# Performance work log

Measured on AMD Instinct MI355X. Metric: run time of the kernel, lower is better.

The kernel has to match this reference:

```python
import jax, jax.numpy as jnp
import numpy as np

SIG_EPS = 0.1
IN_DIM = 256
OUT_DIM = 64


def setup_inputs() -> dict:
    key = jax.random.key(0)
    ks = jax.random.split(key, 6)
    B, S, Q = 32, 512, 512
    return {
        "phi_support": jax.random.normal(ks[0], (B, S, IN_DIM), jnp.float32),
        "y_support": jax.random.normal(ks[1], (B, S, OUT_DIM), jnp.float32),
        "phi_query": jax.random.normal(ks[2], (B, Q, IN_DIM), jnp.float32),
        "y_query": jax.random.normal(ks[3], (B, Q, OUT_DIM), jnp.float32),
        # learned parameters (K init'd to zeros in torch, use small randn for a non-trivial test)
        "K": jax.random.normal(ks[4], (IN_DIM, OUT_DIM), jnp.float32) * 0.02,
        "L_asym": jax.random.normal(ks[5], (IN_DIM, IN_DIM), jnp.float32) * 0.1,
    }


def reference(phi_support, y_support, phi_query, y_query, K, L_asym):
    sig_eps = jnp.float32(SIG_EPS)
    log_sig_eps = jnp.log(sig_eps)
    out_dim = K.shape[1]

    L = L_asym @ L_asym.T  # [I, I]
    # nobs > 0 branch (n_support = 512)
    posterior_L = jnp.einsum('bsi,bsj->bij', phi_support, phi_support) + L[None]  # [B,I,I]
    posterior_L_inv = jnp.linalg.inv(posterior_L)
    rhs = jnp.einsum('bsi,bso->bio', phi_support, y_support) + (L @ K)[None]  # [B,I,O]
    posterior_K = posterior_L_inv @ rhs  # [B,I,O]

    mu_pred = phi_query @ posterior_K  # [B,Q,O]
    # spread_fac = 1 + diag quadratic form phi Linv phi^T  -> [B,Q]
    spread_fac = 1.0 + jnp.einsum('bqi,bij,bqj->bq', phi_query, posterior_L_inv, phi_query)
    eye_eps = jnp.eye(out_dim, dtype=phi_query.dtype) * sig_eps
    sig_pred = spread_fac[..., None, None] * eye_eps  # [B,Q,O,O]

    # predictive_nll: inverse of sig_pred is an exactly scaled identity, so the
    # quadratic form y^T inv(sig_pred) y == ||y||^2 / (spread_fac * sig_eps) (same math)
    diff = y_query - mu_pred
    quadf = jnp.sum(diff * diff, axis=-1) / (spread_fac * sig_eps)  # [B,Q]
    logdet = out_dim * (jnp.log(spread_fac) + log_sig_eps)  # [B,Q]
    predictive_nll = logdet.mean() + quadf.mean()

    return (mu_pred, sig_pred, predictive_nll)
```

## Files before the change

kernel.cpp:

```cpp
#include <hip/hip_runtime.h>
#include <math.h>

#define B 32
#define S 512
#define Q 512
#define I 256
#define O 64
#define SIG_EPS 0.1f
#define LOG_SIG_EPS (-2.3025850929940457f)

#define WS_L 0
#define WS_T1 65536
#define WS_LKT 81920
#define WS_M0 98304
#define WS_M1 2195456
#define WS_RHST 4292608
#define WS_D 4816896
#define WS_SP 5079040
#define WS_NLL 5095424
#define WS_U16 5095488
#define U_PTH 0
#define U_PTL 4194304
#define U_YTH 8388608
#define U_YTL 9437184
#define U_IVH 10485760
#define U_IVL 12582912
#define U_PKH 14680064
#define U_PKL 15204352

#define OUT_MU_ELEMS (B * Q * O)
#define OUT_SIG_ELEMS (B * Q * O * O)
#define OUT_NLL_IDX (OUT_MU_ELEMS + OUT_SIG_ELEMS)

typedef short short8 __attribute__((ext_vector_type(8)));
typedef float f32x4 __attribute__((ext_vector_type(4)));
#define MFMA16(a, b, c) __builtin_amdgcn_mfma_f32_16x16x32_bf16(a, b, c, 0, 0, 0)

__device__ __forceinline__ f32x4 mfma3(short8 ah, short8 al, short8 bh, short8 bl, f32x4 c) {
  c = MFMA16(ah, bh, c);
  c = MFMA16(ah, bl, c);
  c = MFMA16(al, bh, c);
  return c;
}

__device__ __forceinline__ unsigned short f2bf(float x) {
  unsigned int u = __float_as_uint(x);
  return (unsigned short)((u + 0x7fffu + ((u >> 16) & 1u)) >> 16);
}
__device__ __forceinline__ float bf2f(unsigned short h) { return __uint_as_float(((unsigned int)h) << 16); }
__device__ __forceinline__ void split2(float x, unsigned short& h, unsigned short& l) {
  h = f2bf(x);
  l = f2bf(x - bf2f(h));
}
__device__ __forceinline__ void split4(float4 v, uint2& H, uint2& L) {
  unsigned short h0, h1, h2, h3, l0, l1, l2, l3;
  split2(v.x, h0, l0); split2(v.y, h1, l1); split2(v.z, h2, l2); split2(v.w, h3, l3);
  H.x = (unsigned)h0 | ((unsigned)h1 << 16); H.y = (unsigned)h2 | ((unsigned)h3 << 16);
  L.x = (unsigned)l0 | ((unsigned)l1 << 16); L.y = (unsigned)l2 | ((unsigned)l3 << 16);
}
__device__ __forceinline__ void cvt8(const float* p, short8& h8, short8& l8) {
  float4 a = *(const float4*)p;
  float4 b = *(const float4*)(p + 4);
  uint2 H0, L0, H1, L1;
  split4(a, H0, L0); split4(b, H1, L1);
  union { uint2 q[2]; short8 s; } uh, ul;
  uh.q[0] = H0; uh.q[1] = H1; ul.q[0] = L0; ul.q[1] = L1;
  h8 = uh.s; l8 = ul.s;
}
__device__ __forceinline__ short8 ld8(const unsigned short* p) { return *(const short8*)(const void*)p; }

__device__ __forceinline__ void fma4x4(const float4 av, const float4 bv, float acc[4][4]) {
  const float ar[4] = {av.x, av.y, av.z, av.w};
  const float br[4] = {bv.x, bv.y, bv.z, bv.w};
#pragma unroll
  for (int i = 0; i < 4; ++i)
#pragma unroll
    for (int j = 0; j < 4; ++j) acc[i][j] += ar[i] * br[j];
}

__device__ __forceinline__ void load_direct64(float* dst, int ds, const float* src, int ss, int t) {
#pragma unroll
  for (int m = 0; m < 4; ++m) {
    int r = (t >> 4) + 16 * m, c4 = (t & 15) * 4;
    *(float4*)&dst[r * ds + c4] = *(const float4*)&src[(size_t)r * ss + c4];
  }
}
__device__ __forceinline__ void load_trans64(float* dst, int ds, const float* src, int ss, int t) {
#pragma unroll
  for (int m = 0; m < 4; ++m) {
    int r = (t >> 4) + 16 * m, c4 = (t & 15) * 4;
    float4 v = *(const float4*)&src[(size_t)r * ss + c4];
    dst[(c4 + 0) * ds + r] = v.x;
    dst[(c4 + 1) * ds + r] = v.y;
    dst[(c4 + 2) * ds + r] = v.z;
    dst[(c4 + 3) * ds + r] = v.w;
  }
}
template <int SA, int SB>
__device__ __forceinline__ void gemm64(const float* At, const float* Bs, int tr, int tc, float acc[4][4]) {
#pragma unroll 8
  for (int kk = 0; kk < 64; ++kk) {
    float4 a = *(const float4*)&At[kk * SA + tr * 4];
    float4 b = *(const float4*)&Bs[kk * SB + tc * 4];
    fma4x4(a, b, acc);
  }
}

#define SC4(V) V.x *= pivinv; V.y *= pivinv; V.z *= pivinv; V.w *= pivinv
#define UP4(V, R) V.x -= g * R.x; V.y -= g * R.y; V.z -= g * R.z; V.w -= g * R.w

template <int TS>
__device__ void gj64(const float* T, float* rowbuf, float* Dout, int t) {
  int r = t >> 2, q = t & 3;
  int lane = t & 63;
  float4 A0 = *(const float4*)&T[r * TS + q * 16 + 0];
  float4 A1 = *(const float4*)&T[r * TS + q * 16 + 4];
  float4 A2 = *(const float4*)&T[r * TS + q * 16 + 8];
  float4 A3 = *(const float4*)&T[r * TS + q * 16 + 12];
#define IC(c) (((q * 16 + (c)) == r) ? 1.f : 0.f)
  float4 I0 = make_float4(IC(0), IC(1), IC(2), IC(3));
  float4 I1 = make_float4(IC(4), IC(5), IC(6), IC(7));
  float4 I2 = make_float4(IC(8), IC(9), IC(10), IC(11));
  float4 I3 = make_float4(IC(12), IC(13), IC(14), IC(15));
#undef IC
  for (int p = 0; p < 64; ++p) {
    float* RA = rowbuf + (p & 1) * 128;
    float* RI = RA + 64;
    if (r == p) {
      ((float4*)&RA[q * 16])[0] = A0; ((float4*)&RA[q * 16])[1] = A1;
      ((float4*)&RA[q * 16])[2] = A2; ((float4*)&RA[q * 16])[3] = A3;
      ((float4*)&RI[q * 16])[0] = I0; ((float4*)&RI[q * 16])[1] = I1;
      ((float4*)&RI[q * 16])[2] = I2; ((float4*)&RI[q * 16])[3] = I3;
    }
    __syncthreads();
    float pivinv = 1.0f / RA[p];
    int s = p & 15;
    float4 blk = (s < 8) ? ((s < 4) ? A0 : A1) : ((s < 12) ? A2 : A3);
    int sc = s & 3;
    float ap = (sc == 0) ? blk.x : (sc == 1) ? blk.y : (sc == 2) ? blk.z : blk.w;
    float f = __shfl(ap, (lane & ~3) | (p >> 4), 64);
    float4 ra0 = ((const float4*)&RA[q * 16])[0], ra1 = ((const float4*)&RA[q * 16])[1];
    float4 ra2 = ((const float4*)&RA[q * 16])[2], ra3 = ((const float4*)&RA[q * 16])[3];
    float4 ri0 = ((const float4*)&RI[q * 16])[0], ri1 = ((const float4*)&RI[q * 16])[1];
    float4 ri2 = ((const float4*)&RI[q * 16])[2], ri3 = ((const float4*)&RI[q * 16])[3];
    if (r == p) {
      SC4(A0); SC4(A1); SC4(A2); SC4(A3);
      SC4(I0); SC4(I1); SC4(I2); SC4(I3);
    } else {
      float g = f * pivinv;
      UP4(A0, ra0); UP4(A1, ra1); UP4(A2, ra2); UP4(A3, ra3);
      UP4(I0, ri0); UP4(I1, ri1); UP4(I2, ri2); UP4(I3, ri3);
    }
  }
  ((float4*)&Dout[r * 64 + q * 16])[0] = I0;
  ((float4*)&Dout[r * 64 + q * 16])[1] = I1;
  ((float4*)&Dout[r * 64 + q * 16])[2] = I2;
  ((float4*)&Dout[r * 64 + q * 16])[3] = I3;
}

__global__ __launch_bounds__(256) void k_cvt(const float* __restrict__ phi_s, const float* __restrict__ y_s,
                                             unsigned short* __restrict__ PTh, unsigned short* __restrict__ PTl,
                                             unsigned short* __restrict__ YTh, unsigned short* __restrict__ YTl,
                                             float* __restrict__ nllacc) {
  __shared__ unsigned short Hs[64][68];
  __shared__ unsigned short Lo[64][68];
  int blk = blockIdx.x, t = threadIdx.x;
  if (blk == 0 && t == 0) nllacc[0] = 0.f;
  const float* src;
  unsigned short *dh, *dl;
  int sstride;
  if (blk < 1024) {
    int b = blk >> 5, r = blk & 31, ic = r >> 3, sc = r & 7;
    src = phi_s + ((size_t)b * 512 + sc * 64) * 256 + ic * 64;
    sstride = 256;
    size_t d0 = ((size_t)b * 256 + ic * 64) * 512 + sc * 64;
    dh = PTh + d0; dl = PTl + d0;
  } else {
    int qq = blk - 1024, b = qq >> 3, sc = qq & 7;
    src = y_s + ((size_t)b * 512 + sc * 64) * 64;
    sstride = 64;
    size_t d0 = ((size_t)b * 64) * 512 + sc * 64;
    dh = YTh + d0; dl = YTl + d0;
  }
  int c = t & 63, rb = (t >> 6) * 16;
#pragma unroll
  for (int m = 0; m < 16; ++m) {
    int s = rb + m;
    float x = src[(size_t)s * sstride + c];
    unsigned short h, l;
    split2(x, h, l);
    Hs[c][s] = h;
    Lo[c][s] = l;
  }
  __syncthreads();
  int il0 = t >> 4, c4 = (t & 15) * 4;
#pragma unroll
  for (int m = 0; m < 4; ++m) {
    int il = il0 + 16 * m;
    uint2 H, L;
    H.x = (unsigned)Hs[il][c4] | ((unsigned)Hs[il][c4 + 1] << 16);
    H.y = (unsigned)Hs[il][c4 + 2] | ((unsigned)Hs[il][c4 + 3] << 16);
    L.x = (unsigned)Lo[il][c4] | ((unsigned)Lo[il][c4 + 1] << 16);
    L.y = (unsigned)Lo[il][c4 + 2] | ((unsigned)Lo[il][c4 + 3] << 16);
    *(uint2*)&dh[(size_t)il * 512 + c4] = H;
    *(uint2*)&dl[(size_t)il * 512 + c4] = L;
  }
}

__global__ __launch_bounds__(256) void k_pre1(const float* __restrict__ La, const float* __restrict__ Km,
                                              float* __restrict__ Lm, float* __restrict__ T1) {
  __shared__ float sA[16 * 68];
  __shared__ float sB[16 * 68];
  int blk = blockIdx.x, t = threadIdx.x;
  int tr = t >> 4, tc = t & 15;
  float acc[4][4] = {};
  if (blk < 16) {
    int i0 = (blk >> 2) * 64, j0 = (blk & 3) * 64;
    for (int ks = 0; ks < 256; ks += 16) {
      __syncthreads();
#pragma unroll
      for (int m = 0; m < 4; ++m) {
        int r = (t >> 4) + 16 * m, kk = t & 15;
        sA[kk * 68 + r] = La[(size_t)(i0 + r) * 256 + ks + kk];
        sB[kk * 68 + r] = La[(size_t)(j0 + r) * 256 + ks + kk];
      }
      __syncthreads();
#pragma unroll
      for (int kk = 0; kk < 16; ++kk) {
        float4 a = *(const float4*)&sA[kk * 68 + tr * 4];
        float4 bv = *(const float4*)&sB[kk * 68 + tc * 4];
        fma4x4(a, bv, acc);
      }
    }
#pragma unroll
    for (int mi = 0; mi < 4; ++mi) {
      float4 v = {acc[mi][0], acc[mi][1], acc[mi][2], acc[mi][3]};
      *(float4*)&Lm[(size_t)(i0 + tr * 4 + mi) * 256 + j0 + tc * 4] = v;
    }
  } else {
    int i0 = (blk - 16) * 64;
    for (int ks = 0; ks < 256; ks += 16) {
      __syncthreads();
#pragma unroll
      for (int m = 0; m < 4; ++m) {
        int kk = (t >> 6) + 4 * m, c = t & 63;
        sA[kk * 68 + c] = La[(size_t)(ks + kk) * 256 + i0 + c];
        sB[kk * 68 + c] = Km[(size_t)(ks + kk) * 64 + c];
      }
      __syncthreads();
#pragma unroll
      for (int kk = 0; kk < 16; ++kk) {
        float4 a = *(const float4*)&sA[kk * 68 + tr * 4];
        float4 bv = *(const float4*)&sB[kk * 68 + tc * 4];
        fma4x4(a, bv, acc);
      }
    }
#pragma unroll
    for (int mi = 0; mi < 4; ++mi) {
      float4 v = {acc[mi][0], acc[mi][1], acc[mi][2], acc[mi][3]};
      *(float4*)&T1[(size_t)(i0 + tr * 4 + mi) * 64 + tc * 4] = v;
    }
  }
}

__global__ __launch_bounds__(256) void k_gram(
    const unsigned short* __restrict__ PTh, const unsigned short* __restrict__ PTl,
    const unsigned short* __restrict__ YTh, const unsigned short* __restrict__ YTl,
    const float* __restrict__ Lm, const float* __restrict__ La, const float* __restrict__ T1,
    float* __restrict__ M0, float* __restrict__ RHST, float* __restrict__ LKT, float* __restrict__ Dbuf) {
  __shared__ float trbuf[64 * 68];
  __shared__ float rowbuf[256];
  __shared__ float Ws[16 * 64];
  int b = blockIdx.x, y = blockIdx.y, t = threadIdx.x;

  if (y == 14) {
    if (b >= 4) return;
    int i0 = b * 64;
    int tr = t >> 4, tc = t & 15;
    float acc[4][4] = {};
    for (int ks = 0; ks < 256; ks += 16) {
      __syncthreads();
#pragma unroll
      for (int m = 0; m < 4; ++m) {
        trbuf[(t & 15) * 68 + (t >> 4) + 16 * m] = La[(size_t)(i0 + (t >> 4) + 16 * m) * 256 + ks + (t & 15)];
        Ws[((t >> 6) + 4 * m) * 64 + (t & 63)] = T1[(size_t)(ks + (t >> 6) + 4 * m) * 64 + (t & 63)];
      }
      __syncthreads();
#pragma unroll
      for (int kk = 0; kk < 16; ++kk) {
        float4 a = *(const float4*)&trbuf[kk * 68 + tr * 4];
        float4 bv = *(const float4*)&Ws[kk * 64 + tc * 4];
        fma4x4(a, bv, acc);
      }
    }
    __syncthreads();
#pragma unroll
    for (int mi = 0; mi < 4; ++mi)
#pragma unroll
      for (int cj = 0; cj < 4; ++cj) trbuf[(tr * 4 + mi) * 68 + tc * 4 + cj] = acc[mi][cj];
    __syncthreads();
    int rr0 = t >> 4, cc4 = (t & 15) * 4;
#pragma unroll
    for (int m = 0; m < 4; ++m) {
      int rr = rr0 + 16 * m;
      float4 v = {trbuf[(cc4 + 0) * 68 + rr], trbuf[(cc4 + 1) * 68 + rr], trbuf[(cc4 + 2) * 68 + rr],
                  trbuf[(cc4 + 3) * 68 + rr]};
      *(float4*)&LKT[(size_t)rr * 256 + i0 + cc4] = v;
    }
    return;
  }

  const int TIa[14] = {0, 0, 0, 0, 1, 1, 1, 2, 2, 3, 0, 1, 2, 3};
  const int TJa[14] = {0, 1, 2, 3, 1, 2, 3, 2, 3, 3, 0, 0, 0, 0};
  bool isR = (y >= 10);
  int it = TIa[y], jt = TJa[y];
  int i0 = it * 64, j0 = isR ? 0 : jt * 64;
  int lane = t & 63, w = t >> 6, wr = w >> 1, wc = w & 1;
  const unsigned short* Ah = PTh + (size_t)b * 256 * 512;
  const unsigned short* Al = PTl + (size_t)b * 256 * 512;
  const unsigned short* Bh = isR ? (YTh + (size_t)b * 64 * 512) : Ah;
  const unsigned short* Bl = isR ? (YTl + (size_t)b * 64 * 512) : Al;
  int ra0 = i0 + wr * 32 + (lane & 15);
  int rb0 = j0 + wc * 32 + (lane & 15);
  int klane = (lane >> 4) * 8;
  f32x4 acc[2][2] = {};
  for (int ks = 0; ks < 512; ks += 32) {
    int kk = ks + klane;
    short8 a0h = ld8(Ah + (size_t)ra0 * 512 + kk);
    short8 a1h = ld8(Ah + (size_t)(ra0 + 16) * 512 + kk);
    short8 a0l = ld8(Al + (size_t)ra0 * 512 + kk);
    short8 a1l = ld8(Al + (size_t)(ra0 + 16) * 512 + kk);
    short8 b0h = ld8(Bh + (size_t)rb0 * 512 + kk);
    short8 b1h = ld8(Bh + (size_t)(rb0 + 16) * 512 + kk);
    short8 b0l = ld8(Bl + (size_t)rb0 * 512 + kk);
    short8 b1l = ld8(Bl + (size_t)(rb0 + 16) * 512 + kk);
    acc[0][0] = mfma3(a0h, a0l, b0h, b0l, acc[0][0]);
    acc[0][1] = mfma3(a0h, a0l, b1h, b1l, acc[0][1]);
    acc[1][0] = mfma3(a1h, a1l, b0h, b0l, acc[1][0]);
    acc[1][1] = mfma3(a1h, a1l, b1h, b1l, acc[1][1]);
  }
#pragma unroll
  for (int ti = 0; ti < 2; ++ti)
#pragma unroll
    for (int tj = 0; tj < 2; ++tj)
#pragma unroll
      for (int r = 0; r < 4; ++r)
        trbuf[(wr * 32 + ti * 16 + (lane >> 4) * 4 + r) * 68 + wc * 32 + tj * 16 + (lane & 15)] = acc[ti][tj][r];
  __syncthreads();
  int rr0 = t >> 4, cc4 = (t & 15) * 4;
  if (!isR) {
    float* Mb = M0 + (size_t)b * 65536;
    bool d00 = (it == 0 && jt == 0);
#pragma unroll
    for (int m = 0; m < 4; ++m) {
      int rr = rr0 + 16 * m;
      float4 v = *(float4*)&trbuf[rr * 68 + cc4];
      float4 lv = *(const float4*)&Lm[(size_t)(i0 + rr) * 256 + j0 + cc4];
      v.x += lv.x; v.y += lv.y; v.z += lv.z; v.w += lv.w;
      *(float4*)&Mb[(size_t)(i0 + rr) * 256 + j0 + cc4] = v;
      if (d00) *(float4*)&trbuf[rr * 68 + cc4] = v;
    }
    if (it != jt) {
#pragma unroll
      for (int m = 0; m < 4; ++m) {
        int rr = rr0 + 16 * m;
        float4 v = {trbuf[(cc4 + 0) * 68 + rr], trbuf[(cc4 + 1) * 68 + rr], trbuf[(cc4 + 2) * 68 + rr],
                    trbuf[(cc4 + 3) * 68 + rr]};
        float4 lv = *(const float4*)&Lm[(size_t)(j0 + rr) * 256 + i0 + cc4];
        v.x += lv.x; v.y += lv.y; v.z += lv.z; v.w += lv.w;
        *(float4*)&Mb[(size_t)(j0 + rr) * 256 + i0 + cc4] = v;
      }
    }
    if (d00) {
      __syncthreads();
      gj64<68>(trbuf, rowbuf, Dbuf + (size_t)b * 4096, t);
    }
  } else {
#pragma unroll
    for (int m = 0; m < 4; ++m) {
      int rr = rr0 + 16 * m;
      float4 v = {trbuf[(cc4 + 0) * 68 + rr], trbuf[(cc4 + 1) * 68 + rr], trbuf[(cc4 + 2) * 68 + rr],
                  trbuf[(cc4 + 3) * 68 + rr]};
      *(float4*)&RHST[((size_t)b * 64 + rr) * 256 + i0 + cc4] = v;
    }
  }
}

__global__ __launch_bounds__(256) void k_step(const float* __restrict__ Msrc_, float* __restrict__ Mdst_,
                                              float* __restrict__ Dbuf, unsigned short* __restrict__ IVh,
                                              unsigned short* __restrict__ IVl, int kb) {
  __shared__ float shA[64 * 68];
  __shared__ float shB[64 * 64];
  __shared__ float shC[64 * 64];
  __shared__ float shD[64 * 68];
  __shared__ float rowbuf[256];
  int b = blockIdx.x, u = blockIdx.y;
  int i = u >> 2, j = u & 3;
  int t = threadIdx.x;
  int tr = t >> 4, tc = t & 15;
  const float* Ms = Msrc_ + (size_t)b * 65536;
  float* Md = Mdst_ + (size_t)b * 65536;
  const float* Din = Dbuf + (size_t)(kb & 1) * (B * 4096) + (size_t)b * 4096;
  float* Dout = Dbuf + (size_t)((kb + 1) & 1) * (B * 4096) + (size_t)b * 4096;
  bool last = (kb == 3);
  unsigned short* Yh = IVh + (size_t)b * 65536;
  unsigned short* Yl = IVl + (size_t)b * 65536;
  auto STORE = [&](int row, int col, float4 v) {
    if (last) {
      uint2 H, L;
      split4(v, H, L);
      *(uint2*)&Yh[(size_t)row * 256 + col] = H;
      *(uint2*)&Yl[(size_t)row * 256 + col] = L;
    } else {
      *(float4*)&Md[(size_t)row * 256 + col] = v;
    }
  };
  bool ik = (i == kb), jk = (j == kb);
  if (ik && jk) {
#pragma unroll
    for (int m = 0; m < 4; ++m) {
      int r = (t >> 4) + 16 * m, c4 = (t & 15) * 4;
      STORE(kb * 64 + r, kb * 64 + c4, *(const float4*)&Din[r * 64 + c4]);
    }
    return;
  }
  float acc[4][4] = {};
  if (ik) {
    load_trans64(shA, 68, Din, 64, t);
    load_direct64(shB, 64, &Ms[(size_t)(kb * 64) * 256 + j * 64], 256, t);
    __syncthreads();
    gemm64<68, 64>(shA, shB, tr, tc, acc);
#pragma unroll
    for (int mi = 0; mi < 4; ++mi) {
      float4 v = {acc[mi][0], acc[mi][1], acc[mi][2], acc[mi][3]};
      STORE(kb * 64 + tr * 4 + mi, j * 64 + tc * 4, v);
    }
    return;
  }
  if (jk) {
    load_trans64(shA, 68, &Ms[(size_t)(i * 64) * 256 + kb * 64], 256, t);
    load_direct64(shB, 64, Din, 64, t);
    __syncthreads();
    gemm64<68, 64>(shA, shB, tr, tc, acc);
#pragma unroll
    for (int mi = 0; mi < 4; ++mi) {
      float4 v = {-acc[mi][0], -acc[mi][1], -acc[mi][2], -acc[mi][3]};
      STORE(i * 64 + tr * 4 + mi, kb * 64 + tc * 4, v);
    }
    return;
  }
  load_trans64(shA, 68, Din, 64, t);
  load_direct64(shB, 64, &Ms[(size_t)(kb * 64) * 256 + j * 64], 256, t);
  load_trans64(shD, 68, &Ms[(size_t)(i * 64) * 256 + kb * 64], 256, t);
  __syncthreads();
  gemm64<68, 64>(shA, shB, tr, tc, acc);
#pragma unroll
  for (int mi = 0; mi < 4; ++mi) {
    float4 v = {acc[mi][0], acc[mi][1], acc[mi][2], acc[mi][3]};
    *(float4*)&shC[(tr * 4 + mi) * 64 + tc * 4] = v;
  }
  __syncthreads();
  float acc2[4][4] = {};
  gemm64<68, 64>(shD, shC, tr, tc, acc2);
  bool la = (kb < 3) && (i == kb + 1) && (j == kb + 1);
#pragma unroll
  for (int mi = 0; mi < 4; ++mi) {
    size_t off = (size_t)(i * 64 + tr * 4 + mi) * 256 + j * 64 + tc * 4;
    float4 old = *(const float4*)&Ms[off];
    float4 v = {old.x - acc2[mi][0], old.y - acc2[mi][1], old.z - acc2[mi][2], old.w - acc2[mi][3]};
    STORE(i * 64 + tr * 4 + mi, j * 64 + tc * 4, v);
    if (la) *(float4*)&shB[(tr * 4 + mi) * 64 + tc * 4] = v;
  }
  if (la) {
    __syncthreads();
    gj64<64>(shB, rowbuf, Dout, t);
  }
}

__global__ __launch_bounds__(256) void k_postK(const unsigned short* __restrict__ IVh,
                                               const unsigned short* __restrict__ IVl,
                                               const float* __restrict__ RHST, const float* __restrict__ LKT,
                                               unsigned short* __restrict__ PKh, unsigned short* __restrict__ PKl) {
  int b = blockIdx.x, i0 = blockIdx.y * 64, t = threadIdx.x;
  int lane = t & 63, w = t >> 6, wr = w >> 1, wc = w & 1;
  const unsigned short* Ah = IVh + (size_t)b * 65536;
  const unsigned short* Al = IVl + (size_t)b * 65536;
  int ra0 = i0 + wr * 32 + (lane & 15);
  int ob0 = wc * 32 + (lane & 15);
  int klane = (lane >> 4) * 8;
  f32x4 acc[2][2] = {};
  for (int ks = 0; ks < 256; ks += 32) {
    int kk = ks + klane;
    short8 a0h = ld8(Ah + (size_t)ra0 * 256 + kk);
    short8 a1h = ld8(Ah + (size_t)(ra0 + 16) * 256 + kk);
    short8 a0l = ld8(Al + (size_t)ra0 * 256 + kk);
    short8 a1l = ld8(Al + (size_t)(ra0 + 16) * 256 + kk);
    short8 bh[2], bl[2];
#pragma unroll
    for (int s = 0; s < 2; ++s) {
      int o = ob0 + s * 16;
      float g[8];
      float4 g0 = *(const float4*)&RHST[((size_t)b * 64 + o) * 256 + kk];
      float4 g1 = *(const float4*)&RHST[((size_t)b * 64 + o) * 256 + kk + 4];
      float4 l0 = *(const float4*)&LKT[(size_t)o * 256 + kk];
      float4 l1 = *(const float4*)&LKT[(size_t)o * 256 + kk + 4];
      g[0] = g0.x + l0.x; g[1] = g0.y + l0.y; g[2] = g0.z + l0.z; g[3] = g0.w + l0.w;
      g[4] = g1.x + l1.x; g[5] = g1.y + l1.y; g[6] = g1.z + l1.z; g[7] = g1.w + l1.w;
      cvt8(g, bh[s], bl[s]);
    }
    acc[0][0] = mfma3(a0h, a0l, bh[0], bl[0], acc[0][0]);
    acc[0][1] = mfma3(a0h, a0l, bh[1], bl[1], acc[0][1]);
    acc[1][0] = mfma3(a1h, a1l, bh[0], bl[0], acc[1][0]);
    acc[1][1] = mfma3(a1h, a1l, bh[1], bl[1], acc[1][1]);
  }
#pragma unroll
  for (int ti = 0; ti < 2; ++ti)
#pragma unroll
    for (int tj = 0; tj < 2; ++tj) {
      int ib = i0 + wr * 32 + ti * 16 + (lane >> 4) * 4;
      int o = wc * 32 + tj * 16 + (lane & 15);
      float4 v = {acc[ti][tj][0], acc[ti][tj][1], acc[ti][tj][2], acc[ti][tj][3]};
      uint2 H, L;
      split4(v, H, L);
      *(uint2*)&PKh[((size_t)b * 64 + o) * 256 + ib] = H;
      *(uint2*)&PKl[((size_t)b * 64 + o) * 256 + ib] = L;
    }
}

__global__ __launch_bounds__(256) void k_musp(const float* __restrict__ phi_q,
                                              const unsigned short* __restrict__ IVh,
                                              const unsigned short* __restrict__ IVl,
                                              const unsigned short* __restrict__ PKh,
                                              const unsigned short* __restrict__ PKl, float* __restrict__ mu,
                                              float* __restrict__ spread) {
  int b = blockIdx.x, qb = blockIdx.y * 64, t = threadIdx.x;
  int lane = t & 63, w = t >> 6;
  int qs = qb + w * 16;
  int qlane = qs + (lane & 15);
  int klane = (lane >> 4) * 8;
  const float* Pq = phi_q + (size_t)b * 512 * 256;
  short8 ah[8], al[8];
#pragma unroll
  for (int k8 = 0; k8 < 8; ++k8) cvt8(&Pq[(size_t)qlane * 256 + k8 * 32 + klane], ah[k8], al[k8]);
  const unsigned short* Kh = PKh + (size_t)b * 64 * 256;
  const unsigned short* Kl = PKl + (size_t)b * 64 * 256;
#pragma unroll
  for (int ot = 0; ot < 4; ++ot) {
    f32x4 acc = {};
    int orow = ot * 16 + (lane & 15);
#pragma unroll
    for (int k8 = 0; k8 < 8; ++k8) {
      short8 bh = ld8(Kh + (size_t)orow * 256 + k8 * 32 + klane);
      short8 bl = ld8(Kl + (size_t)orow * 256 + k8 * 32 + klane);
      acc = mfma3(ah[k8], al[k8], bh, bl, acc);
    }
#pragma unroll
    for (int r = 0; r < 4; ++r)
      mu[((size_t)b * 512 + qs + (lane >> 4) * 4 + r) * 64 + ot * 16 + (lane & 15)] = acc[r];
  }
  const unsigned short* Vh = IVh + (size_t)b * 65536;
  const unsigned short* Vl = IVl + (size_t)b * 65536;
  float rs[4] = {0.f, 0.f, 0.f, 0.f};
  for (int jt = 0; jt < 16; ++jt) {
    f32x4 acc = {};
    int jrow = jt * 16 + (lane & 15);
#pragma unroll
    for (int k8 = 0; k8 < 8; ++k8) {
      short8 bh = ld8(Vh + (size_t)jrow * 256 + k8 * 32 + klane);
      short8 bl = ld8(Vl + (size_t)jrow * 256 + k8 * 32 + klane);
      acc = mfma3(ah[k8], al[k8], bh, bl, acc);
    }
#pragma unroll
    for (int r = 0; r < 4; ++r) {
      int q = qs + (lane >> 4) * 4 + r;
      rs[r] += acc[r] * Pq[(size_t)q * 256 + jt * 16 + (lane & 15)];
    }
  }
#pragma unroll
  for (int off = 1; off < 16; off <<= 1)
#pragma unroll
    for (int r = 0; r < 4; ++r) rs[r] += __shfl_xor(rs[r], off);
  if ((lane & 15) == 0) {
#pragma unroll
    for (int r = 0; r < 4; ++r) spread[(size_t)b * 512 + qs + (lane >> 4) * 4 + r] = 1.0f + rs[r];
  }
}

__global__ __launch_bounds__(256) void k_signll(const float* __restrict__ spread, float4* __restrict__ sig,
                                                const float* __restrict__ yq, const float* __restrict__ mu,
                                                float* __restrict__ nllacc) {
  int t = threadIdx.x;
  if (blockIdx.x < 65536) {
    size_t idx = (size_t)blockIdx.x * 256 + t;
    int p4 = (int)(idx & 15);
    int o = (int)((idx >> 4) & 63);
    size_t bq = idx >> 10;
    float sv = spread[bq] * SIG_EPS;
    float4 v;
    v.x = (p4 * 4 + 0 == o) ? sv : 0.f;
    v.y = (p4 * 4 + 1 == o) ? sv : 0.f;
    v.z = (p4 * 4 + 2 == o) ? sv : 0.f;
    v.w = (p4 * 4 + 3 == o) ? sv : 0.f;
    sig[idx] = v;
  } else {
    int bq = (blockIdx.x - 65536) * 256 + t;
    float sp = spread[bq];
    const float4* yv = (const float4*)(yq + (size_t)bq * 64);
    const float4* mv = (const float4*)(mu + (size_t)bq * 64);
    float ssd = 0.f;
#pragma unroll
    for (int i = 0; i < 16; ++i) {
      float4 a = yv[i], b = mv[i];
      float dx = a.x - b.x, dy = a.y - b.y, dz = a.z - b.z, dw = a.w - b.w;
      ssd += dx * dx + dy * dy + dz * dz + dw * dw;
    }
    float quadf = ssd / (sp * SIG_EPS);
    float ld = 64.0f * (logf(sp) + LOG_SIG_EPS);
    float val = (ld + quadf) * (1.0f / 16384.0f);
#pragma unroll
    for (int off = 32; off; off >>= 1) val += __shfl_down(val, off);
    if ((t & 63) == 0) atomicAdd(nllacc, val);
  }
}

__global__ void k_fin(const float* __restrict__ nllacc, float* __restrict__ out) {
  if (threadIdx.x == 0 && blockIdx.x == 0) out[0] = nllacc[0];
}

extern "C" void kernel_launch(void* const* d_in, const int* in_sizes, int n_in, void* d_out, int out_size,
                              void* d_ws, size_t ws_size, hipStream_t stream) {
  const float* phi_s = (const float*)d_in[0];
  const float* y_s = (const float*)d_in[1];
  const float* phi_q = (const float*)d_in[2];
  const float* y_q = (const float*)d_in[3];
  const float* Km = (const float*)d_in[4];
  const float* La = (const float*)d_in[5];

  float* ws = (float*)d_ws;
  float* Lm = ws + WS_L;
  float* T1 = ws + WS_T1;
  float* LKT = ws + WS_LKT;
  float* M0 = ws + WS_M0;
  float* M1 = ws + WS_M1;
  float* RHST = ws + WS_RHST;
  float* Dbuf = ws + WS_D;
  float* spread = ws + WS_SP;
  float* nllacc = ws + WS_NLL;
  unsigned short* u16b = (unsigned short*)(ws + WS_U16);
  unsigned short* PTh = u16b + U_PTH;
  unsigned short* PTl = u16b + U_PTL;
  unsigned short* YTh = u16b + U_YTH;
  unsigned short* YTl = u16b + U_YTL;
  unsigned short* IVh = u16b + U_IVH;
  unsigned short* IVl = u16b + U_IVL;
  unsigned short* PKh = u16b + U_PKH;
  unsigned short* PKl = u16b + U_PKL;

  float* out_mu = (float*)d_out;
  float* out_sig = out_mu + OUT_MU_ELEMS;
  float* out_nll = out_mu + OUT_NLL_IDX;

  k_cvt<<<1280, 256, 0, stream>>>(phi_s, y_s, PTh, PTl, YTh, YTl, nllacc);
  k_pre1<<<20, 256, 0, stream>>>(La, Km, Lm, T1);
  k_gram<<<dim3(B, 15), 256, 0, stream>>>(PTh, PTl, YTh, YTl, Lm, La, T1, M0, RHST, LKT, Dbuf);
  k_step<<<dim3(B, 16), 256, 0, stream>>>(M0, M1, Dbuf, IVh, IVl, 0);
  k_step<<<dim3(B, 16), 256, 0, stream>>>(M1, M0, Dbuf, IVh, IVl, 1);
  k_step<<<dim3(B, 16), 256, 0, stream>>>(M0, M1, Dbuf, IVh, IVl, 2);
  k_step<<<dim3(B, 16), 256, 0, stream>>>(M1, M0, Dbuf, IVh, IVl, 3);
  k_postK<<<dim3(B, 4), 256, 0, stream>>>(IVh, IVl, RHST, LKT, PKh, PKl);
  k_musp<<<dim3(B, 8), 256, 0, stream>>>(phi_q, IVh, IVl, PKh, PKl, out_mu, spread);
  k_signll<<<65600, 256, 0, stream>>>(spread, (float4*)out_sig, y_q, out_mu, nllacc);
  k_fin<<<1, 64, 0, stream>>>(nllacc, out_nll);
}
```

Baseline: 336.0 us.

## Fuse all stages into one cooperative persistent kernel with grid syncs

Replaces the chain of eleven kernel launches with a single cooperative kernel of 256 persistent blocks that loops over work units for each phase, separated by grid-wide syncs. It also merges mu/spread computation with sigma writing and the NLL reduction into one tail phase, so the spread buffer and the separate sigma/NLL kernel and finalization pass are removed. Kernel-launch gaps go away, but each phase now runs on only 256 blocks, which can limit parallelism for the large sigma write and the conversion phase. A multi-launch fallback is kept for devices without cooperative launch support.

New measurement: 351.6 us. +4.6%, slower.

```diff
diff --git a/kernel.cpp b/kernel.cpp
--- a/kernel.cpp
+++ b/kernel.cpp
@@ -1,5 +1,8 @@
 #include <hip/hip_runtime.h>
+#include <hip/hip_cooperative_groups.h>
 #include <math.h>
+
+namespace cg = cooperative_groups;
 
 #define B 32
 #define S 512
@@ -16,9 +19,7 @@
 #define WS_M1 2195456
 #define WS_RHST 4292608
 #define WS_D 4816896
-#define WS_SP 5079040
-#define WS_NLL 5095424
-#define WS_U16 5095488
+#define WS_U16 5079040
 #define U_PTH 0
 #define U_PTL 4194304
 #define U_YTH 8388608
@@ -35,6 +36,14 @@
 typedef short short8 __attribute__((ext_vector_type(8)));
 typedef float f32x4 __attribute__((ext_vector_type(4)));
 #define MFMA16(a, b, c) __builtin_amdgcn_mfma_f32_16x16x32_bf16(a, b, c, 0, 0, 0)
+
+struct Params {
+  const float *phi_s, *y_s, *phi_q, *y_q, *Km, *La;
+  float *Lm, *T1, *LKT, *M0, *M1, *RHST, *Dbuf;
+  unsigned short *PTh, *PTl, *YTh, *YTl, *IVh, *IVl, *PKh, *PKl;
+  float *mu, *nll;
+  float4 *sig;
+};
 
 __device__ __forceinline__ f32x4 mfma3(short8 ah, short8 al, short8 bh, short8 bl, f32x4 c) {
   c = MFMA16(ah, bh, c);
@@ -134,9 +143,9 @@
     }
     __syncthreads();
     float pivinv = 1.0f / RA[p];
-    int s = p & 15;
-    float4 blk = (s < 8) ? ((s < 4) ? A0 : A1) : ((s < 12) ? A2 : A3);
-    int sc = s & 3;
+    int sidx = p & 15;
+    float4 blk = (sidx < 8) ? ((sidx < 4) ? A0 : A1) : ((sidx < 12) ? A2 : A3);
+    int sc = sidx & 3;
     float ap = (sc == 0) ? blk.x : (sc == 1) ? blk.y : (sc == 2) ? blk.z : blk.w;
     float f = __shfl(ap, (lane & ~3) | (p >> 4), 64);
     float4 ra0 = ((const float4*)&RA[q * 16])[0], ra1 = ((const float4*)&RA[q * 16])[1];
@@ -158,122 +167,111 @@
   ((float4*)&Dout[r * 64 + q * 16])[3] = I3;
 }
 
-__global__ __launch_bounds__(256) void k_cvt(const float* __restrict__ phi_s, const float* __restrict__ y_s,
-                                             unsigned short* __restrict__ PTh, unsigned short* __restrict__ PTl,
-                                             unsigned short* __restrict__ YTh, unsigned short* __restrict__ YTl,
-                                             float* __restrict__ nllacc) {
-  __shared__ unsigned short Hs[64][68];
-  __shared__ unsigned short Lo[64][68];
-  int blk = blockIdx.x, t = threadIdx.x;
-  if (blk == 0 && t == 0) nllacc[0] = 0.f;
-  const float* src;
-  unsigned short *dh, *dl;
-  int sstride;
-  if (blk < 1024) {
-    int b = blk >> 5, r = blk & 31, ic = r >> 3, sc = r & 7;
-    src = phi_s + ((size_t)b * 512 + sc * 64) * 256 + ic * 64;
-    sstride = 256;
-    size_t d0 = ((size_t)b * 256 + ic * 64) * 512 + sc * 64;
-    dh = PTh + d0; dl = PTl + d0;
+__device__ void phase0_unit(const Params& p, int w, int t, float* smem) {
+  if (w < 1280) {
+    unsigned short* Hs = (unsigned short*)smem;
+    unsigned short* Lo = Hs + 64 * 68;
+    const float* src;
+    unsigned short *dh, *dl;
+    int sstride;
+    if (w < 1024) {
+      int b = w >> 5, r = w & 31, ic = r >> 3, sc = r & 7;
+      src = p.phi_s + ((size_t)b * 512 + sc * 64) * 256 + ic * 64;
+      sstride = 256;
+      size_t d0 = ((size_t)b * 256 + ic * 64) * 512 + sc * 64;
+      dh = p.PTh + d0; dl = p.PTl + d0;
+    } else {
+      int qq = w - 1024, b = qq >> 3, sc = qq & 7;
+      src = p.y_s + ((size_t)b * 512 + sc * 64) * 64;
+      sstride = 64;
+      size_t d0 = ((size_t)b * 64) * 512 + sc * 64;
+      dh = p.YTh + d0; dl = p.YTl + d0;
+    }
+    int c = t & 63, rb = (t >> 6) * 16;
+#pragma unroll
+    for (int m = 0; m < 16; ++m) {
+      int s = rb + m;
+      float x = src[(size_t)s * sstride + c];
+      unsigned short h, l;
+      split2(x, h, l);
+      Hs[c * 68 + s] = h;
+      Lo[c * 68 + s] = l;
+    }
+    __syncthreads();
+    int il0 = t >> 4, c4 = (t & 15) * 4;
+#pragma unroll
+    for (int m = 0; m < 4; ++m) {
+      int il = il0 + 16 * m;
+      uint2 H, L;
+      H.x = (unsigned)Hs[il * 68 + c4] | ((unsigned)Hs[il * 68 + c4 + 1] << 16);
+      H.y = (unsigned)Hs[il * 68 + c4 + 2] | ((unsigned)Hs[il * 68 + c4 + 3] << 16);
+      L.x = (unsigned)Lo[il * 68 + c4] | ((unsigned)Lo[il * 68 + c4 + 1] << 16);
+      L.y = (unsigned)Lo[il * 68 + c4 + 2] | ((unsigned)Lo[il * 68 + c4 + 3] << 16);
+      *(uint2*)&dh[(size_t)il * 512 + c4] = H;
+      *(uint2*)&dl[(size_t)il * 512 + c4] = L;
+    }
   } else {
-    int qq = blk - 1024, b = qq >> 3, sc = qq & 7;
-    src = y_s + ((size_t)b * 512 + sc * 64) * 64;
-    sstride = 64;
-    size_t d0 = ((size_t)b * 64) * 512 + sc * 64;
-    dh = YTh + d0; dl = YTl + d0;
-  }
-  int c = t & 63, rb = (t >> 6) * 16;
-#pragma unroll
-  for (int m = 0; m < 16; ++m) {
-    int s = rb + m;
-    float x = src[(size_t)s * sstride + c];
-    unsigned short h, l;
-    split2(x, h, l);
-    Hs[c][s] = h;
-    Lo[c][s] = l;
-  }
-  __syncthreads();
-  int il0 = t >> 4, c4 = (t & 15) * 4;
-#pragma unroll
-  for (int m = 0; m < 4; ++m) {
-    int il = il0 + 16 * m;
-    uint2 H, L;
-    H.x = (unsigned)Hs[il][c4] | ((unsigned)Hs[il][c4 + 1] << 16);
-    H.y = (unsigned)Hs[il][c4 + 2] | ((unsigned)Hs[il][c4 + 3] << 16);
-    L.x = (unsigned)Lo[il][c4] | ((unsigned)Lo[il][c4 + 1] << 16);
-    L.y = (unsigned)Lo[il][c4 + 2] | ((unsigned)Lo[il][c4 + 3] << 16);
-    *(uint2*)&dh[(size_t)il * 512 + c4] = H;
-    *(uint2*)&dl[(size_t)il * 512 + c4] = L;
-  }
-}
-
-__global__ __launch_bounds__(256) void k_pre1(const float* __restrict__ La, const float* __restrict__ Km,
-                                              float* __restrict__ Lm, float* __restrict__ T1) {
-  __shared__ float sA[16 * 68];
-  __shared__ float sB[16 * 68];
-  int blk = blockIdx.x, t = threadIdx.x;
-  int tr = t >> 4, tc = t & 15;
-  float acc[4][4] = {};
-  if (blk < 16) {
-    int i0 = (blk >> 2) * 64, j0 = (blk & 3) * 64;
-    for (int ks = 0; ks < 256; ks += 16) {
-      __syncthreads();
-#pragma unroll
-      for (int m = 0; m < 4; ++m) {
-        int r = (t >> 4) + 16 * m, kk = t & 15;
-        sA[kk * 68 + r] = La[(size_t)(i0 + r) * 256 + ks + kk];
-        sB[kk * 68 + r] = La[(size_t)(j0 + r) * 256 + ks + kk];
+    int blk2 = w - 1280;
+    float* sA = smem;
+    float* sB = smem + 1088;
+    int tr = t >> 4, tc = t & 15;
+    float acc[4][4] = {};
+    if (blk2 < 16) {
+      int i0 = (blk2 >> 2) * 64, j0 = (blk2 & 3) * 64;
+      for (int ks = 0; ks < 256; ks += 16) {
+        __syncthreads();
+#pragma unroll
+        for (int m = 0; m < 4; ++m) {
+          int r = (t >> 4) + 16 * m, kk = t & 15;
+          sA[kk * 68 + r] = p.La[(size_t)(i0 + r) * 256 + ks + kk];
+          sB[kk * 68 + r] = p.La[(size_t)(j0 + r) * 256 + ks + kk];
+        }
+        __syncthreads();
+#pragma unroll
+        for (int kk = 0; kk < 16; ++kk) {
+          float4 a = *(const float4*)&sA[kk * 68 + tr * 4];
+          float4 bv = *(const float4*)&sB[kk * 68 + tc * 4];
+          fma4x4(a, bv, acc);
+        }
       }
-      __syncthreads();
-#pragma unroll
-      for (int kk = 0; kk < 16; ++kk) {
-        float4 a = *(const float4*)&sA[kk * 68 + tr * 4];
-        float4 bv = *(const float4*)&sB[kk * 68 + tc * 4];
-        fma4x4(a, bv, acc);
+#pragma unroll
+      for (int mi = 0; mi < 4; ++mi) {
+        float4 v = {acc[mi][0], acc[mi][1], acc[mi][2], acc[mi][3]};
+        *(float4*)&p.Lm[(size_t)(i0 + tr * 4 + mi) * 256 + j0 + tc * 4] = v;
       }
-    }
-#pragma unroll
-    for (int mi = 0; mi < 4; ++mi) {
-      float4 v = {acc[mi][0], acc[mi][1], acc[mi][2], acc[mi][3]};
-      *(float4*)&Lm[(size_t)(i0 + tr * 4 + mi) * 256 + j0 + tc * 4] = v;
-    }
-  } else {
-    int i0 = (blk - 16) * 64;
-    for (int ks = 0; ks < 256; ks += 16) {
-      __syncthreads();
-#pragma unroll
-      for (int m = 0; m < 4; ++m) {
-        int kk = (t >> 6) + 4 * m, c = t & 63;
-        sA[kk * 68 + c] = La[(size_t)(ks + kk) * 256 + i0 + c];
-        sB[kk * 68 + c] = Km[(size_t)(ks + kk) * 64 + c];
+    } else {
+      int i0 = (blk2 - 16) * 64;
+      for (int ks = 0; ks < 256; ks += 16) {
+        __syncthreads();
+#pragma unroll
+        for (int m = 0; m < 4; ++m) {
+          int kk = (t >> 6) + 4 * m, c = t & 63;
+          sA[kk * 68 + c] = p.La[(size_t)(ks + kk) * 256 + i0 + c];
+          sB[kk * 68 + c] = p.Km[(size_t)(ks + kk) * 64 + c];
+        }
+        __syncthreads();
+#pragma unroll
+        for (int kk = 0; kk < 16; ++kk) {
+          float4 a = *(const float4*)&sA[kk * 68 + tr * 4];
+          float4 bv = *(const float4*)&sB[kk * 68 + tc * 4];
+          fma4x4(a, bv, acc);
+        }
       }
-      __syncthreads();
-#pragma unroll
-      for (int kk = 0; kk < 16; ++kk) {
-        float4 a = *(const float4*)&sA[kk * 68 + tr * 4];
-        float4 bv = *(const float4*)&sB[kk * 68 + tc * 4];
-        fma4x4(a, bv, acc);
+#pragma unroll
+      for (int mi = 0; mi < 4; ++mi) {
+        float4 v = {acc[mi][0], acc[mi][1], acc[mi][2], acc[mi][3]};
+        *(float4*)&p.T1[(size_t)(i0 + tr * 4 + mi) * 64 + tc * 4] = v;
       }
     }
-#pragma unroll
-    for (int mi = 0; mi < 4; ++mi) {
-      float4 v = {acc[mi][0], acc[mi][1], acc[mi][2], acc[mi][3]};
-      *(float4*)&T1[(size_t)(i0 + tr * 4 + mi) * 64 + tc * 4] = v;
-    }
-  }
-}
-
-__global__ __launch_bounds__(256) void k_gram(
-    const unsigned short* __restrict__ PTh, const unsigned short* __restrict__ PTl,
-    const unsigned short* __restrict__ YTh, const unsigned short* __restrict__ YTl,
-    const float* __restrict__ Lm, const float* __restrict__ La, const float* __restrict__ T1,
-    float* __restrict__ M0, float* __restrict__ RHST, float* __restrict__ LKT, float* __restrict__ Dbuf) {
-  __shared__ float trbuf[64 * 68];
-  __shared__ float rowbuf[256];
-  __shared__ float Ws[16 * 64];
-  int b = blockIdx.x, y = blockIdx.y, t = threadIdx.x;
-
-  if (y == 14) {
+  }
+}
+
+__device__ void gram_unit(const Params& p, int b, int u, int t, float* smem) {
+  float* trbuf = smem;
+  float* Ws = smem + 4352;
+  float* rowb = smem + 12800;
+  if (u == 15) return;
+  if (u == 14) {
     if (b >= 4) return;
     int i0 = b * 64;
     int tr = t >> 4, tc = t & 15;
@@ -282,8 +280,8 @@
       __syncthreads();
 #pragma unroll
       for (int m = 0; m < 4; ++m) {
-        trbuf[(t & 15) * 68 + (t >> 4) + 16 * m] = La[(size_t)(i0 + (t >> 4) + 16 * m) * 256 + ks + (t & 15)];
-        Ws[((t >> 6) + 4 * m) * 64 + (t & 63)] = T1[(size_t)(ks + (t >> 6) + 4 * m) * 64 + (t & 63)];
+        trbuf[(t & 15) * 68 + (t >> 4) + 16 * m] = p.La[(size_t)(i0 + (t >> 4) + 16 * m) * 256 + ks + (t & 15)];
+        Ws[((t >> 6) + 4 * m) * 64 + (t & 63)] = p.T1[(size_t)(ks + (t >> 6) + 4 * m) * 64 + (t & 63)];
       }
       __syncthreads();
 #pragma unroll
@@ -305,21 +303,20 @@
       int rr = rr0 + 16 * m;
       float4 v = {trbuf[(cc4 + 0) * 68 + rr], trbuf[(cc4 + 1) * 68 + rr], trbuf[(cc4 + 2) * 68 + rr],
                   trbuf[(cc4 + 3) * 68 + rr]};
-      *(float4*)&LKT[(size_t)rr * 256 + i0 + cc4] = v;
+      *(float4*)&p.LKT[(size_t)rr * 256 + i0 + cc4] = v;
     }
     return;
   }
-
   const int TIa[14] = {0, 0, 0, 0, 1, 1, 1, 2, 2, 3, 0, 1, 2, 3};
   const int TJa[14] = {0, 1, 2, 3, 1, 2, 3, 2, 3, 3, 0, 0, 0, 0};
-  bool isR = (y >= 10);
-  int it = TIa[y], jt = TJa[y];
+  bool isR = (u >= 10);
+  int it = TIa[u], jt = TJa[u];
   int i0 = it * 64, j0 = isR ? 0 : jt * 64;
   int lane = t & 63, w = t >> 6, wr = w >> 1, wc = w & 1;
-  const unsigned short* Ah = PTh + (size_t)b * 256 * 512;
-  const unsigned short* Al = PTl + (size_t)b * 256 * 512;
-  const unsigned short* Bh = isR ? (YTh + (size_t)b * 64 * 512) : Ah;
-  const unsigned short* Bl = isR ? (YTl + (size_t)b * 64 * 512) : Al;
+  const unsigned short* Ah = p.PTh + (size_t)b * 256 * 512;
+  const unsigned short* Al = p.PTl + (size_t)b * 256 * 512;
+  const unsigned short* Bh = isR ? (p.YTh + (size_t)b * 64 * 512) : Ah;
+  const unsigned short* Bl = isR ? (p.YTl + (size_t)b * 64 * 512) : Al;
   int ra0 = i0 + wr * 32 + (lane & 15);
   int rb0 = j0 + wc * 32 + (lane & 15);
   int klane = (lane >> 4) * 8;
@@ -349,13 +346,13 @@
   __syncthreads();
   int rr0 = t >> 4, cc4 = (t & 15) * 4;
   if (!isR) {
-    float* Mb = M0 + (size_t)b * 65536;
+    float* Mb = p.M0 + (size_t)b * 65536;
     bool d00 = (it == 0 && jt == 0);
 #pragma unroll
     for (int m = 0; m < 4; ++m) {
       int rr = rr0 + 16 * m;
       float4 v = *(float4*)&trbuf[rr * 68 + cc4];
-      float4 lv = *(const float4*)&Lm[(size_t)(i0 + rr) * 256 + j0 + cc4];
+      float4 lv = *(const float4*)&p.Lm[(size_t)(i0 + rr) * 256 + j0 + cc4];
       v.x += lv.x; v.y += lv.y; v.z += lv.z; v.w += lv.w;
       *(float4*)&Mb[(size_t)(i0 + rr) * 256 + j0 + cc4] = v;
       if (d00) *(float4*)&trbuf[rr * 68 + cc4] = v;
@@ -366,14 +363,14 @@
         int rr = rr0 + 16 * m;
         float4 v = {trbuf[(cc4 + 0) * 68 + rr], trbuf[(cc4 + 1) * 68 + rr], trbuf[(cc4 + 2) * 68 + rr],
                     trbuf[(cc4 + 3) * 68 + rr]};
-        float4 lv = *(const float4*)&Lm[(size_t)(j0 + rr) * 256 + i0 + cc4];
+        float4 lv = *(const float4*)&p.Lm[(size_t)(j0 + rr) * 256 + i0 + cc4];
         v.x += lv.x; v.y += lv.y; v.z += lv.z; v.w += lv.w;
         *(float4*)&Mb[(size_t)(j0 + rr) * 256 + i0 + cc4] = v;
       }
     }
     if (d00) {
       __syncthreads();
-      gj64<68>(trbuf, rowbuf, Dbuf + (size_t)b * 4096, t);
+      gj64<68>(trbuf, rowb, p.Dbuf + (size_t)b * 4096, t);
     }
   } else {
 #pragma unroll
@@ -381,30 +378,25 @@
       int rr = rr0 + 16 * m;
       float4 v = {trbuf[(cc4 + 0) * 68 + rr], trbuf[(cc4 + 1) * 68 + rr], trbuf[(cc4 + 2) * 68 + rr],
                   trbuf[(cc4 + 3) * 68 + rr]};
-      *(float4*)&RHST[((size_t)b * 64 + rr) * 256 + i0 + cc4] = v;
-    }
-  }
-}
-
-__global__ __launch_bounds__(256) void k_step(const float* __restrict__ Msrc_, float* __restrict__ Mdst_,
-                                              float* __restrict__ Dbuf, unsigned short* __restrict__ IVh,
-                                              unsigned short* __restrict__ IVl, int kb) {
-  __shared__ float shA[64 * 68];
-  __shared__ float shB[64 * 64];
-  __shared__ float shC[64 * 64];
-  __shared__ float shD[64 * 68];
-  __shared__ float rowbuf[256];
-  int b = blockIdx.x, u = blockIdx.y;
+      *(float4*)&p.RHST[((size_t)b * 64 + rr) * 256 + i0 + cc4] = v;
+    }
+  }
+}
+
+__device__ void st_unit(const Params& p, int b, int u, int kb, int t, float* smem) {
+  float* shA = smem;
+  float* shB = smem + 4352;
+  float* shD = smem + 8448;
+  float* rowb = smem + 12800;
   int i = u >> 2, j = u & 3;
-  int t = threadIdx.x;
   int tr = t >> 4, tc = t & 15;
-  const float* Ms = Msrc_ + (size_t)b * 65536;
-  float* Md = Mdst_ + (size_t)b * 65536;
-  const float* Din = Dbuf + (size_t)(kb & 1) * (B * 4096) + (size_t)b * 4096;
-  float* Dout = Dbuf + (size_t)((kb + 1) & 1) * (B * 4096) + (size_t)b * 4096;
+  const float* Ms = ((kb & 1) ? p.M1 : p.M0) + (size_t)b * 65536;
+  float* Md = ((kb & 1) ? p.M0 : p.M1) + (size_t)b * 65536;
+  const float* Din = p.Dbuf + (size_t)(kb & 1) * (B * 4096) + (size_t)b * 4096;
+  float* Dout = p.Dbuf + (size_t)((kb + 1) & 1) * (B * 4096) + (size_t)b * 4096;
   bool last = (kb == 3);
-  unsigned short* Yh = IVh + (size_t)b * 65536;
-  unsigned short* Yl = IVl + (size_t)b * 65536;
+  unsigned short* Yh = p.IVh + (size_t)b * 65536;
+  unsigned short* Yl = p.IVl + (size_t)b * 65536;
   auto STORE = [&](int row, int col, float4 v) {
     if (last) {
       uint2 H, L;
@@ -422,69 +414,68 @@
       int r = (t >> 4) + 16 * m, c4 = (t & 15) * 4;
       STORE(kb * 64 + r, kb * 64 + c4, *(const float4*)&Din[r * 64 + c4]);
     }
-    return;
-  }
-  float acc[4][4] = {};
-  if (ik) {
+  } else if (ik) {
+    float acc[4][4] = {};
     load_trans64(shA, 68, Din, 64, t);
     load_direct64(shB, 64, &Ms[(size_t)(kb * 64) * 256 + j * 64], 256, t);
     __syncthreads();
     gemm64<68, 64>(shA, shB, tr, tc, acc);
+    __syncthreads();
 #pragma unroll
     for (int mi = 0; mi < 4; ++mi) {
       float4 v = {acc[mi][0], acc[mi][1], acc[mi][2], acc[mi][3]};
       STORE(kb * 64 + tr * 4 + mi, j * 64 + tc * 4, v);
     }
-    return;
-  }
-  if (jk) {
+  } else if (jk) {
+    float acc[4][4] = {};
     load_trans64(shA, 68, &Ms[(size_t)(i * 64) * 256 + kb * 64], 256, t);
     load_direct64(shB, 64, Din, 64, t);
     __syncthreads();
     gemm64<68, 64>(shA, shB, tr, tc, acc);
+    __syncthreads();
 #pragma unroll
     for (int mi = 0; mi < 4; ++mi) {
       float4 v = {-acc[mi][0], -acc[mi][1], -acc[mi][2], -acc[mi][3]};
       STORE(i * 64 + tr * 4 + mi, kb * 64 + tc * 4, v);
     }
-    return;
-  }
-  load_trans64(shA, 68, Din, 64, t);
-  load_direct64(shB, 64, &Ms[(size_t)(kb * 64) * 256 + j * 64], 256, t);
-  load_trans64(shD, 68, &Ms[(size_t)(i * 64) * 256 + kb * 64], 256, t);
-  __syncthreads();
-  gemm64<68, 64>(shA, shB, tr, tc, acc);
-#pragma unroll
-  for (int mi = 0; mi < 4; ++mi) {
-    float4 v = {acc[mi][0], acc[mi][1], acc[mi][2], acc[mi][3]};
-    *(float4*)&shC[(tr * 4 + mi) * 64 + tc * 4] = v;
-  }
-  __syncthreads();
-  float acc2[4][4] = {};
-  gemm64<68, 64>(shD, shC, tr, tc, acc2);
-  bool la = (kb < 3) && (i == kb + 1) && (j == kb + 1);
-#pragma unroll
-  for (int mi = 0; mi < 4; ++mi) {
-    size_t off = (size_t)(i * 64 + tr * 4 + mi) * 256 + j * 64 + tc * 4;
-    float4 old = *(const float4*)&Ms[off];
-    float4 v = {old.x - acc2[mi][0], old.y - acc2[mi][1], old.z - acc2[mi][2], old.w - acc2[mi][3]};
-    STORE(i * 64 + tr * 4 + mi, j * 64 + tc * 4, v);
-    if (la) *(float4*)&shB[(tr * 4 + mi) * 64 + tc * 4] = v;
-  }
-  if (la) {
-    __syncthreads();
-    gj64<64>(shB, rowbuf, Dout, t);
-  }
-}
-
-__global__ __launch_bounds__(256) void k_postK(const unsigned short* __restrict__ IVh,
-                                               const unsigned short* __restrict__ IVl,
-                                               const float* __restrict__ RHST, const float* __restrict__ LKT,
-                                               unsigned short* __restrict__ PKh, unsigned short* __restrict__ PKl) {
-  int b = blockIdx.x, i0 = blockIdx.y * 64, t = threadIdx.x;
+  } else {
+    float acc[4][4] = {};
+    load_trans64(shA, 68, Din, 64, t);
+    load_direct64(shB, 64, &Ms[(size_t)(kb * 64) * 256 + j * 64], 256, t);
+    load_trans64(shD, 68, &Ms[(size_t)(i * 64) * 256 + kb * 64], 256, t);
+    __syncthreads();
+    gemm64<68, 64>(shA, shB, tr, tc, acc);
+    __syncthreads();
+#pragma unroll
+    for (int mi = 0; mi < 4; ++mi) {
+      float4 v = {acc[mi][0], acc[mi][1], acc[mi][2], acc[mi][3]};
+      *(float4*)&shB[(tr * 4 + mi) * 64 + tc * 4] = v;
+    }
+    __syncthreads();
+    float acc2[4][4] = {};
+    gemm64<68, 64>(shD, shB, tr, tc, acc2);
+    bool la = (kb < 3) && (i == kb + 1) && (j == kb + 1);
+    if (la) __syncthreads();
+#pragma unroll
+    for (int mi = 0; mi < 4; ++mi) {
+      size_t off = (size_t)(i * 64 + tr * 4 + mi) * 256 + j * 64 + tc * 4;
+      float4 old = *(const float4*)&Ms[off];
+      float4 v = {old.x - acc2[mi][0], old.y - acc2[mi][1], old.z - acc2[mi][2], old.w - acc2[mi][3]};
+      STORE(i * 64 + tr * 4 + mi, j * 64 + tc * 4, v);
+      if (la) *(float4*)&shB[(tr * 4 + mi) * 64 + tc * 4] = v;
+    }
+    if (la) {
+      __syncthreads();
+      gj64<64>(shB, rowb, Dout, t);
+    }
+  }
+}
+
+__device__ void postk_unit(const Params& p, int b, int u, int t) {
+  int i0 = u * 64;
   int lane = t & 63, w = t >> 6, wr = w >> 1, wc = w & 1;
-  const unsigned short* Ah = IVh + (size_t)b * 65536;
-  const unsigned short* Al = IVl + (size_t)b * 65536;
+  const unsigned short* Ah = p.IVh + (size_t)b * 65536;
+  const unsigned short* Al = p.IVl + (size_t)b * 65536;
   int ra0 = i0 + wr * 32 + (lane & 15);
   int ob0 = wc * 32 + (lane & 15);
   int klane = (lane >> 4) * 8;
@@ -497,16 +488,16 @@
     short8 a1l = ld8(Al + (size_t)(ra0 + 16) * 256 + kk);
     short8 bh[2], bl[2];
 #pragma unroll
-    for (int s = 0; s < 2; ++s) {
-      int o = ob0 + s * 16;
+    for (int sjj = 0; sjj < 2; ++sjj) {
+      int o = ob0 + sjj * 16;
       float g[8];
-      float4 g0 = *(const float4*)&RHST[((size_t)b * 64 + o) * 256 + kk];
-      float4 g1 = *(const float4*)&RHST[((size_t)b * 64 + o) * 256 + kk + 4];
-      float4 l0 = *(const float4*)&LKT[(size_t)o * 256 + kk];
-      float4 l1 = *(const float4*)&LKT[(size_t)o * 256 + kk + 4];
+      float4 g0 = *(const float4*)&p.RHST[((size_t)b * 64 + o) * 256 + kk];
+      float4 g1 = *(const float4*)&p.RHST[((size_t)b * 64 + o) * 256 + kk + 4];
+      float4 l0 = *(const float4*)&p.LKT[(size_t)o * 256 + kk];
+      float4 l1 = *(const float4*)&p.LKT[(size_t)o * 256 + kk + 4];
       g[0] = g0.x + l0.x; g[1] = g0.y + l0.y; g[2] = g0.z + l0.z; g[3] = g0.w + l0.w;
       g[4] = g1.x + l1.x; g[5] = g1.y + l1.y; g[6] = g1.z + l1.z; g[7] = g1.w + l1.w;
-      cvt8(g, bh[s], bl[s]);
+      cvt8(g, bh[sjj], bl[sjj]);
     }
     acc[0][0] = mfma3(a0h, a0l, bh[0], bl[0], acc[0][0]);
     acc[0][1] = mfma3(a0h, a0l, bh[1], bl[1], acc[0][1]);
@@ -522,30 +513,31 @@
       float4 v = {acc[ti][tj][0], acc[ti][tj][1], acc[ti][tj][2], acc[ti][tj][3]};
       uint2 H, L;
       split4(v, H, L);
-      *(uint2*)&PKh[((size_t)b * 64 + o) * 256 + ib] = H;
-      *(uint2*)&PKl[((size_t)b * 64 + o) * 256 + ib] = L;
-    }
-}
-
-__global__ __launch_bounds__(256) void k_musp(const float* __restrict__ phi_q,
-                                              const unsigned short* __restrict__ IVh,
-                                              const unsigned short* __restrict__ IVl,
-                                              const unsigned short* __restrict__ PKh,
-                                              const unsigned short* __restrict__ PKl, float* __restrict__ mu,
-                                              float* __restrict__ spread) {
-  int b = blockIdx.x, qb = blockIdx.y * 64, t = threadIdx.x;
+      *(uint2*)&p.PKh[((size_t)b * 64 + o) * 256 + ib] = H;
+      *(uint2*)&p.PKl[((size_t)b * 64 + o) * 256 + ib] = L;
+    }
+}
+
+__device__ void tail_unit(const Params& p, int b, int qb, int t, float* smem) {
+  float (*red)[4] = (float(*)[4])smem;
+  float* spf = smem + 128;
   int lane = t & 63, w = t >> 6;
-  int qs = qb + w * 16;
-  int qlane = qs + (lane & 15);
+  int hs = w >> 1;
+  int s = w & 1;
+  int rows16 = qb + hs * 16;
+  int qlane = rows16 + (lane & 15);
   int klane = (lane >> 4) * 8;
-  const float* Pq = phi_q + (size_t)b * 512 * 256;
+  const float* Pq = p.phi_q + (size_t)b * 512 * 256;
   short8 ah[8], al[8];
 #pragma unroll
   for (int k8 = 0; k8 < 8; ++k8) cvt8(&Pq[(size_t)qlane * 256 + k8 * 32 + klane], ah[k8], al[k8]);
-  const unsigned short* Kh = PKh + (size_t)b * 64 * 256;
-  const unsigned short* Kl = PKl + (size_t)b * 64 * 256;
-#pragma unroll
-  for (int ot = 0; ot < 4; ++ot) {
+
+  const unsigned short* Kh = p.PKh + (size_t)b * 16384;
+  const unsigned short* Kl = p.PKl + (size_t)b * 16384;
+  float ssdr[4] = {0.f, 0.f, 0.f, 0.f};
+#pragma unroll
+  for (int oi = 0; oi < 2; ++oi) {
+    int ot = s * 2 + oi;
     f32x4 acc = {};
     int orow = ot * 16 + (lane & 15);
 #pragma unroll
@@ -555,13 +547,19 @@
       acc = mfma3(ah[k8], al[k8], bh, bl, acc);
     }
 #pragma unroll
-    for (int r = 0; r < 4; ++r)
-      mu[((size_t)b * 512 + qs + (lane >> 4) * 4 + r) * 64 + ot * 16 + (lane & 15)] = acc[r];
-  }
-  const unsigned short* Vh = IVh + (size_t)b * 65536;
-  const unsigned short* Vl = IVl + (size_t)b * 65536;
+    for (int r = 0; r < 4; ++r) {
+      int qrow = rows16 + (lane >> 4) * 4 + r;
+      int o = ot * 16 + (lane & 15);
+      float m = acc[r];
+      p.mu[((size_t)b * 512 + qrow) * 64 + o] = m;
+      float d = p.y_q[((size_t)b * 512 + qrow) * 64 + o] - m;
+      ssdr[r] += d * d;
+    }
+  }
+  const unsigned short* Vh = p.IVh + (size_t)b * 65536;
+  const unsigned short* Vl = p.IVl + (size_t)b * 65536;
   float rs[4] = {0.f, 0.f, 0.f, 0.f};
-  for (int jt = 0; jt < 16; ++jt) {
+  for (int jt = s * 8; jt < s * 8 + 8; ++jt) {
     f32x4 acc = {};
     int jrow = jt * 16 + (lane & 15);
 #pragma unroll
@@ -572,103 +570,158 @@
     }
 #pragma unroll
     for (int r = 0; r < 4; ++r) {
-      int q = qs + (lane >> 4) * 4 + r;
-      rs[r] += acc[r] * Pq[(size_t)q * 256 + jt * 16 + (lane & 15)];
+      int qrow = rows16 + (lane >> 4) * 4 + r;
+      rs[r] += acc[r] * Pq[(size_t)qrow * 256 + jt * 16 + (lane & 15)];
     }
   }
 #pragma unroll
   for (int off = 1; off < 16; off <<= 1)
 #pragma unroll
-    for (int r = 0; r < 4; ++r) rs[r] += __shfl_xor(rs[r], off);
+    for (int r = 0; r < 4; ++r) {
+      rs[r] += __shfl_xor(rs[r], off);
+      ssdr[r] += __shfl_xor(ssdr[r], off);
+    }
   if ((lane & 15) == 0) {
 #pragma unroll
-    for (int r = 0; r < 4; ++r) spread[(size_t)b * 512 + qs + (lane >> 4) * 4 + r] = 1.0f + rs[r];
-  }
-}
-
-__global__ __launch_bounds__(256) void k_signll(const float* __restrict__ spread, float4* __restrict__ sig,
-                                                const float* __restrict__ yq, const float* __restrict__ mu,
-                                                float* __restrict__ nllacc) {
-  int t = threadIdx.x;
-  if (blockIdx.x < 65536) {
-    size_t idx = (size_t)blockIdx.x * 256 + t;
-    int p4 = (int)(idx & 15);
-    int o = (int)((idx >> 4) & 63);
-    size_t bq = idx >> 10;
-    float sv = spread[bq] * SIG_EPS;
+    for (int r = 0; r < 4; ++r) {
+      int rloc = hs * 16 + (lane >> 4) * 4 + r;
+      red[rloc][s] = rs[r];
+      red[rloc][2 + s] = ssdr[r];
+    }
+  }
+  __syncthreads();
+  if (w == 0) {
+    float val = 0.f;
+    if (t < 32) {
+      float sp = 1.f + red[t][0] + red[t][1];
+      spf[t] = sp;
+      float ssd = red[t][2] + red[t][3];
+      val = (64.f * (logf(sp) + LOG_SIG_EPS) + ssd / (sp * SIG_EPS)) * (1.0f / 16384.0f);
+    }
+#pragma unroll
+    for (int off = 32; off; off >>= 1) val += __shfl_down(val, off);
+    if (t == 0) atomicAdd(p.nll, val);
+  }
+  __syncthreads();
+  size_t base = ((size_t)b * 512 + qb) * 1024;
+#pragma unroll 4
+  for (int it = 0; it < 128; ++it) {
+    int idx = it * 256 + t;
+    int rloc = idx >> 10;
+    int o = (idx >> 4) & 63;
+    int p4 = idx & 15;
+    float sv = spf[rloc] * SIG_EPS;
     float4 v;
     v.x = (p4 * 4 + 0 == o) ? sv : 0.f;
     v.y = (p4 * 4 + 1 == o) ? sv : 0.f;
     v.z = (p4 * 4 + 2 == o) ? sv : 0.f;
     v.w = (p4 * 4 + 3 == o) ? sv : 0.f;
-    sig[idx] = v;
-  } else {
-    int bq = (blockIdx.x - 65536) * 256 + t;
-    float sp = spread[bq];
-    const float4* yv = (const float4*)(yq + (size_t)bq * 64);
-    const float4* mv = (const float4*)(mu + (size_t)bq * 64);
-    float ssd = 0.f;
-#pragma unroll
-    for (int i = 0; i < 16; ++i) {
-      float4 a = yv[i], b = mv[i];
-      float dx = a.x - b.x, dy = a.y - b.y, dz = a.z - b.z, dw = a.w - b.w;
-      ssd += dx * dx + dy * dy + dz * dz + dw * dw;
-    }
-    float quadf = ssd / (sp * SIG_EPS);
-    float ld = 64.0f * (logf(sp) + LOG_SIG_EPS);
-    float val = (ld + quadf) * (1.0f / 16384.0f);
-#pragma unroll
-    for (int off = 32; off; off >>= 1) val += __shfl_down(val, off);
-    if ((t & 63) == 0) atomicAdd(nllacc, val);
-  }
-}
-
-__global__ void k_fin(const float* __restrict__ nllacc, float* __restrict__ out) {
-  if (threadIdx.x == 0 && blockIdx.x == 0) out[0] = nllacc[0];
+    p.sig[base + idx] = v;
+  }
+}
+
+__global__ __launch_bounds__(256) void k_all(Params p) {
+  cg::grid_group grid = cg::this_grid();
+  __shared__ float smem[13056];
+  int g = blockIdx.x, t = threadIdx.x;
+  if (g == 0 && t == 0) p.nll[0] = 0.f;
+  for (int w = g; w < 1300; w += 256) {
+    __syncthreads();
+    phase0_unit(p, w, t, smem);
+  }
+  __threadfence();
+  grid.sync();
+  for (int w = g; w < 512; w += 256) {
+    __syncthreads();
+    gram_unit(p, w >> 4, w & 15, t, smem);
+  }
+  __threadfence();
+  grid.sync();
+  for (int kb = 0; kb < 4; ++kb) {
+    for (int w = g; w < 512; w += 256) {
+      __syncthreads();
+      st_unit(p, w >> 4, w & 15, kb, t, smem);
+    }
+    __threadfence();
+    grid.sync();
+  }
+  for (int w = g; w < 128; w += 256) postk_unit(p, w >> 2, w & 3, t);
+  __threadfence();
+  grid.sync();
+  for (int w = g; w < 512; w += 256) {
+    __syncthreads();
+    tail_unit(p, w >> 4, (w & 15) * 32, t, smem);
+  }
+}
+
+__global__ __launch_bounds__(256) void k_p0(Params p) {
+  __shared__ float smem[13056];
+  if (blockIdx.x == 0 && threadIdx.x == 0) p.nll[0] = 0.f;
+  phase0_unit(p, blockIdx.x, threadIdx.x, smem);
+}
+__global__ __launch_bounds__(256) void k_gramw(Params p) {
+  __shared__ float smem[13056];
+  gram_unit(p, blockIdx.x >> 4, blockIdx.x & 15, threadIdx.x, smem);
+}
+__global__ __launch_bounds__(256) void k_stw(Params p, int kb) {
+  __shared__ float smem[13056];
+  st_unit(p, blockIdx.x >> 4, blockIdx.x & 15, kb, threadIdx.x, smem);
+}
+__global__ __launch_bounds__(256) void k_postkw(Params p) {
+  postk_unit(p, blockIdx.x >> 2, blockIdx.x & 3, threadIdx.x);
+}
+__global__ __launch_bounds__(256) void k_tailw(Params p) {
+  __shared__ float smem[13056];
+  tail_unit(p, blockIdx.x >> 4, (blockIdx.x & 15) * 32, threadIdx.x, smem);
 }
 
 extern "C" void kernel_launch(void* const* d_in, const int* in_sizes, int n_in, void* d_out, int out_size,
                               void* d_ws, size_t ws_size, hipStream_t stream) {
-  const float* phi_s = (const float*)d_in[0];
-  const float* y_s = (const float*)d_in[1];
-  const float* phi_q = (const float*)d_in[2];
-  const float* y_q = (const float*)d_in[3];
-  const float* Km = (const float*)d_in[4];
-  const float* La = (const float*)d_in[5];
-
   float* ws = (float*)d_ws;
-  float* Lm = ws + WS_L;
-  float* T1 = ws + WS_T1;
-  float* LKT = ws + WS_LKT;
-  float* M0 = ws + WS_M0;
-  float* M1 = ws + WS_M1;
-  float* RHST = ws + WS_RHST;
-  float* Dbuf = ws + WS_D;
-  float* spread = ws + WS_SP;
-  float* nllacc = ws + WS_NLL;
   unsigned short* u16b = (unsigned short*)(ws + WS_U16);
-  unsigned short* PTh = u16b + U_PTH;
-  unsigned short* PTl = u16b + U_PTL;
-  unsigned short* YTh = u16b + U_YTH;
-  unsigned short* YTl = u16b + U_YTL;
-  unsigned short* IVh = u16b + U_IVH;
-  unsigned short* IVl = u16b + U_IVL;
-  unsigned short* PKh = u16b + U_PKH;
-  unsigned short* PKl = u16b + U_PKL;
-
   float* out_mu = (float*)d_out;
-  float* out_sig = out_mu + OUT_MU_ELEMS;
-  float* out_nll = out_mu + OUT_NLL_IDX;
-
-  k_cvt<<<1280, 256, 0, stream>>>(phi_s, y_s, PTh, PTl, YTh, YTl, nllacc);
-  k_pre1<<<20, 256, 0, stream>>>(La, Km, Lm, T1);
-  k_gram<<<dim3(B, 15), 256, 0, stream>>>(PTh, PTl, YTh, YTl, Lm, La, T1, M0, RHST, LKT, Dbuf);
-  k_step<<<dim3(B, 16), 256, 0, stream>>>(M0, M1, Dbuf, IVh, IVl, 0);
-  k_step<<<dim3(B, 16), 256, 0, stream>>>(M1, M0, Dbuf, IVh, IVl, 1);
-  k_step<<<dim3(B, 16), 256, 0, stream>>>(M0, M1, Dbuf, IVh, IVl, 2);
-  k_step<<<dim3(B, 16), 256, 0, stream>>>(M1, M0, Dbuf, IVh, IVl, 3);
-  k_postK<<<dim3(B, 4), 256, 0, stream>>>(IVh, IVl, RHST, LKT, PKh, PKl);
-  k_musp<<<dim3(B, 8), 256, 0, stream>>>(phi_q, IVh, IVl, PKh, PKl, out_mu, spread);
-  k_signll<<<65600, 256, 0, stream>>>(spread, (float4*)out_sig, y_q, out_mu, nllacc);
-  k_fin<<<1, 64, 0, stream>>>(nllacc, out_nll);
-}
+
+  Params p;
+  p.phi_s = (const float*)d_in[0];
+  p.y_s = (const float*)d_in[1];
+  p.phi_q = (const float*)d_in[2];
+  p.y_q = (const float*)d_in[3];
+  p.Km = (const float*)d_in[4];
+  p.La = (const float*)d_in[5];
+  p.Lm = ws + WS_L;
+  p.T1 = ws + WS_T1;
+  p.LKT = ws + WS_LKT;
+  p.M0 = ws + WS_M0;
+  p.M1 = ws + WS_M1;
+  p.RHST = ws + WS_RHST;
+  p.Dbuf = ws + WS_D;
+  p.PTh = u16b + U_PTH;
+  p.PTl = u16b + U_PTL;
+  p.YTh = u16b + U_YTH;
+  p.YTl = u16b + U_YTL;
+  p.IVh = u16b + U_IVH;
+  p.IVl = u16b + U_IVL;
+  p.PKh = u16b + U_PKH;
+  p.PKl = u16b + U_PKL;
+  p.mu = out_mu;
+  p.sig = (float4*)(out_mu + OUT_MU_ELEMS);
+  p.nll = out_mu + OUT_NLL_IDX;
+
+  int dev = 0;
+  hipGetDevice(&dev);
+  int coop = 0;
+  hipDeviceGetAttribute(&coop, hipDeviceAttributeCooperativeLaunch, dev);
+  int maxb = 0;
+  hipOccupancyMaxActiveBlocksPerMultiprocessor(&maxb, (const void*)k_all, 256, 0);
+
+  if (coop && maxb >= 1) {
+    void* kargs[1] = {(void*)&p};
+    hipLaunchCooperativeKernel((const void*)k_all, dim3(256, 1, 1), dim3(256, 1, 1), kargs, 0, stream);
+  } else {
+    k_p0<<<1300, 256, 0, stream>>>(p);
+    k_gramw<<<512, 256, 0, stream>>>(p);
+    for (int kb = 0; kb < 4; ++kb) k_stw<<<512, 256, 0, stream>>>(p, kb);
+    k_postkw<<<128, 256, 0, stream>>>(p);
+    k_tailw<<<512, 256, 0, stream>>>(p);
+  }
+}
```
